# Optimization experiments

Measured on AMD Instinct MI355X. Metric: run time of the kernel, lower is better.

The kernel has to match this reference:

```python
import jax, jax.numpy as jnp
import numpy as np

GAMMA = 1.0

def setup_inputs() -> dict:
    key = jax.random.key(0)
    k1, k2 = jax.random.split(key)
    pred = jax.random.normal(k1, (8, 2048, 8), dtype=jnp.float32)
    target = jax.random.normal(k2, (8, 2048, 8), dtype=jnp.float32)
    return {"pred": pred, "target": target}

def reference(pred, target):
    # pairwise squared distances dist[b,i,j] = sum_f (pred[b,i,f]-target[b,j,f])^2
    # computed as ||p||^2 + ||t||^2 - 2 p.t to avoid materializing (B,L,L,F)
    p2 = jnp.sum(pred * pred, axis=-1)            # (B, L)
    t2 = jnp.sum(target * target, axis=-1)        # (B, L)
    pt = jnp.einsum('bif,bjf->bij', pred, target) # (B, L, L)
    distances = p2[:, :, None] + t2[:, None, :] - 2.0 * pt
    # soft-min over target positions: -gamma * logsumexp(-d/gamma)
    min_distances = -GAMMA * jax.nn.logsumexp(-distances / GAMMA, axis=-1)
    return jnp.mean(min_distances)
```

## Files before the change

kernel.cpp:

```cpp
#include <hip/hip_runtime.h>
#include <math.h>

#define BATCH 8
#define LEN   2048
#define FEAT  8
#define MROWS 64
#define THREADS 1024
#define JW    (LEN / 4)
#define NCHUNK (JW / 16)
#define NBLK  (BATCH * (LEN / MROWS))
#define LOG2E 1.4426950408889634f
#define LN2   0.6931471805599453f

typedef _Float16 f16x8 __attribute__((ext_vector_type(8)));
typedef float    f32x4 __attribute__((ext_vector_type(4)));

__device__ __forceinline__ float exp2_hw(float x) {
    float d; asm("v_exp_f32 %0, %1" : "=v"(d) : "v"(x)); return d;
}
__device__ __forceinline__ float log2_hw(float x) {
    float d; asm("v_log_f32 %0, %1" : "=v"(d) : "v"(x)); return d;
}

template <bool ATOMIC>
__global__ __launch_bounds__(THREADS, 4) void dtw_mfma(
    const float* __restrict__ pred, const float* __restrict__ target,
    float* __restrict__ partial_or_out)
{
    __shared__ f16x8 s_t16[LEN];
    __shared__ float s_mt2[LEN];

    const int tid = threadIdx.x;
    const int b   = blockIdx.x / (LEN / MROWS);
    const int rs  = blockIdx.x % (LEN / MROWS);
    const int w   = tid >> 6;
    const int rg  = w >> 2;
    const int jq  = w & 3;
    const int ln  = tid & 63;
    const int i0  = rs * MROWS + rg * 16;

    const float4* t4 = (const float4*)(target + (size_t)b * LEN * FEAT);
    #pragma unroll
    for (int u = 0; u < LEN / THREADS; ++u) {
        const int jj = u * THREADS + tid;
        float4 ta = t4[(size_t)jj * 2];
        float4 tb = t4[(size_t)jj * 2 + 1];
        f16x8 h;
        h[0] = (_Float16)ta.x; h[1] = (_Float16)ta.y;
        h[2] = (_Float16)ta.z; h[3] = (_Float16)ta.w;
        h[4] = (_Float16)tb.x; h[5] = (_Float16)tb.y;
        h[6] = (_Float16)tb.z; h[7] = (_Float16)tb.w;
        float t2 = 0.f;
        #pragma unroll
        for (int e = 0; e < 8; ++e) { float f = (float)h[e]; t2 += f * f; }
        s_t16[jj] = h;
        s_mt2[jj] = -LOG2E * t2;
    }

    f16x8 afrag;
    #pragma unroll
    for (int e = 0; e < 8; ++e) afrag[e] = (_Float16)0.f;
    float mp2_lane = 0.f;
    if (ln < 16) {
        const float4* p4 =
            (const float4*)(pred + ((size_t)b * LEN + i0 + ln) * FEAT);
        float4 a = p4[0], c = p4[1];
        f16x8 h;
        h[0] = (_Float16)a.x; h[1] = (_Float16)a.y;
        h[2] = (_Float16)a.z; h[3] = (_Float16)a.w;
        h[4] = (_Float16)c.x; h[5] = (_Float16)c.y;
        h[6] = (_Float16)c.z; h[7] = (_Float16)c.w;
        float p2 = 0.f;
        #pragma unroll
        for (int e = 0; e < 8; ++e) { float f = (float)h[e]; p2 += f * f; }
        #pragma unroll
        for (int e = 0; e < 8; ++e) afrag[e] = h[e] * (_Float16)2.0f;
        mp2_lane = -LOG2E * p2;
    }
    float m2r[4];
    #pragma unroll
    for (int r = 0; r < 4; ++r)
        m2r[r] = __shfl(mp2_lane, (ln >> 4) * 4 + r);

    __syncthreads();

    const int jbase = jq * JW;
    f32x4 acc = {0.f, 0.f, 0.f, 0.f};
    #pragma unroll 4
    for (int ch = 0; ch < NCHUNK; ++ch) {
        const int j0 = jbase + ch * 16;
        f16x8 bfrag;
        #pragma unroll
        for (int e = 0; e < 8; ++e) bfrag[e] = (_Float16)0.f;
        if (ln < 16) bfrag = s_t16[j0 + ln];
        float mt2c = s_mt2[j0 + (ln & 15)];
        f32x4 S = __builtin_amdgcn_mfma_f32_16x16x32_f16(
            afrag, bfrag, (f32x4){0.f, 0.f, 0.f, 0.f}, 0, 0, 0);
        #pragma unroll
        for (int r = 0; r < 4; ++r) {
            float x = fmaf(S[r], LOG2E, m2r[r] + mt2c);
            acc[r] += exp2_hw(x);
        }
    }

    #pragma unroll
    for (int m = 1; m < 16; m <<= 1) {
        #pragma unroll
        for (int r = 0; r < 4; ++r) acc[r] += __shfl_xor(acc[r], m);
    }

    __syncthreads();
    float* s_red = (float*)s_t16;
    if ((ln & 15) == 0) {
        #pragma unroll
        for (int r = 0; r < 4; ++r) {
            const int row = rg * 16 + (ln >> 4) * 4 + r;
            s_red[row * 4 + jq] = acc[r];
        }
    }
    __syncthreads();
    if (tid < 64) {
        float s = s_red[tid * 4] + s_red[tid * 4 + 1]
                + s_red[tid * 4 + 2] + s_red[tid * 4 + 3];
        float v = log2_hw(s);
        v += __shfl_xor(v, 1);
        v += __shfl_xor(v, 2);
        v += __shfl_xor(v, 4);
        v += __shfl_xor(v, 8);
        v += __shfl_xor(v, 16);
        v += __shfl_xor(v, 32);
        if (tid == 0) {
            float tot = -LN2 * v;
            if (ATOMIC) {
                atomicAdd(partial_or_out, tot * (1.0f / (BATCH * LEN)));
            } else {
                partial_or_out[blockIdx.x] = tot;
            }
        }
    }
}

__global__ __launch_bounds__(256) void dtw_reduce(
    const float* __restrict__ partial, float* __restrict__ out)
{
    __shared__ float s_w[4];
    const int tid = threadIdx.x;
    float v = partial[tid];
    v += __shfl_xor(v, 1);
    v += __shfl_xor(v, 2);
    v += __shfl_xor(v, 4);
    v += __shfl_xor(v, 8);
    v += __shfl_xor(v, 16);
    v += __shfl_xor(v, 32);
    if ((tid & 63) == 0) s_w[tid >> 6] = v;
    __syncthreads();
    if (tid == 0)
        out[0] = (s_w[0] + s_w[1] + s_w[2] + s_w[3]) * (1.0f / (BATCH * LEN));
}

extern "C" void kernel_launch(void* const* d_in, const int* in_sizes, int n_in,
                              void* d_out, int out_size, void* d_ws, size_t ws_size,
                              hipStream_t stream) {
    const float* pred   = (const float*)d_in[0];
    const float* target = (const float*)d_in[1];
    float* out = (float*)d_out;

    if (ws_size >= NBLK * sizeof(float)) {
        float* partial = (float*)d_ws;
        dtw_mfma<false><<<NBLK, THREADS, 0, stream>>>(pred, target, partial);
        dtw_reduce<<<1, 256, 0, stream>>>(partial, out);
    } else {
        hipMemsetAsync(d_out, 0, sizeof(float), stream);
        dtw_mfma<true><<<NBLK, THREADS, 0, stream>>>(pred, target, out);
    }
}
```

Before: 16.04 us.

## Reuse each target fragment across two MFMAs and factor the pred norm out of the exponent

Each wave now covers 32 pred rows with two MFMAs sharing one B fragment, over an eighth of the target range instead of a quarter. The 2*log2e scale is folded into the fp16 A fragment, so the per-element exponent argument drops from an fma plus add to a single add. The per-row pred-norm term is instead subtracted once after the log. It also fully unrolls the chunk loop and uses a dedicated shared reduction buffer, which removes one barrier. The risk is more registers and less stable results, since the exp2 argument no longer includes the -p2 shift and could overflow for rows with large norms.

```diff
diff --git a/kernel.cpp b/kernel.cpp
--- a/kernel.cpp
+++ b/kernel.cpp
@@ -6,11 +6,12 @@
 #define FEAT  8
 #define MROWS 64
 #define THREADS 1024
-#define JW    (LEN / 4)
-#define NCHUNK (JW / 16)
+#define JO    (LEN / 8)
+#define NCHUNK (JO / 16)
 #define NBLK  (BATCH * (LEN / MROWS))
 #define LOG2E 1.4426950408889634f
 #define LN2   0.6931471805599453f
+#define P2S   (2.0f * LOG2E)
 
 typedef _Float16 f16x8 __attribute__((ext_vector_type(8)));
 typedef float    f32x4 __attribute__((ext_vector_type(4)));
@@ -29,15 +30,19 @@
 {
     __shared__ f16x8 s_t16[LEN];
     __shared__ float s_mt2[LEN];
+    __shared__ float s_red[MROWS * 8];
+    __shared__ float s_qp[MROWS];
 
     const int tid = threadIdx.x;
     const int b   = blockIdx.x / (LEN / MROWS);
     const int rs  = blockIdx.x % (LEN / MROWS);
     const int w   = tid >> 6;
-    const int rg  = w >> 2;
-    const int jq  = w & 3;
+    const int rg  = w >> 3;
+    const int jo  = w & 7;
     const int ln  = tid & 63;
-    const int i0  = rs * MROWS + rg * 16;
+    const int col = ln & 15;
+    const int g   = ln >> 4;
+    const int i0  = rs * MROWS + rg * 32;
 
     const float4* t4 = (const float4*)(target + (size_t)b * LEN * FEAT);
     #pragma unroll
@@ -57,72 +62,80 @@
         s_mt2[jj] = -LOG2E * t2;
     }
 
-    f16x8 afrag;
+    f16x8 afrag0, afrag1;
     #pragma unroll
-    for (int e = 0; e < 8; ++e) afrag[e] = (_Float16)0.f;
-    float mp2_lane = 0.f;
-    if (ln < 16) {
-        const float4* p4 =
-            (const float4*)(pred + ((size_t)b * LEN + i0 + ln) * FEAT);
-        float4 a = p4[0], c = p4[1];
-        f16x8 h;
-        h[0] = (_Float16)a.x; h[1] = (_Float16)a.y;
-        h[2] = (_Float16)a.z; h[3] = (_Float16)a.w;
-        h[4] = (_Float16)c.x; h[5] = (_Float16)c.y;
-        h[6] = (_Float16)c.z; h[7] = (_Float16)c.w;
-        float p2 = 0.f;
+    for (int e = 0; e < 8; ++e) { afrag0[e] = (_Float16)0.f;
+                                  afrag1[e] = (_Float16)0.f; }
+    float qp0 = 0.f, qp1 = 0.f;
+    {
+        const float* pb = pred + ((size_t)b * LEN + i0 + col) * FEAT;
+        const float4* pA = (const float4*)pb;
+        const float4* pB = (const float4*)(pb + 16 * FEAT);
+        float4 a0 = pA[0], c0 = pA[1], a1 = pB[0], c1 = pB[1];
+        float f0[8] = {a0.x, a0.y, a0.z, a0.w, c0.x, c0.y, c0.z, c0.w};
+        float f1[8] = {a1.x, a1.y, a1.z, a1.w, c1.x, c1.y, c1.z, c1.w};
+        f16x8 r0, r1;
+        float e0 = 0.f, e1 = 0.f;
         #pragma unroll
-        for (int e = 0; e < 8; ++e) { float f = (float)h[e]; p2 += f * f; }
-        #pragma unroll
-        for (int e = 0; e < 8; ++e) afrag[e] = h[e] * (_Float16)2.0f;
-        mp2_lane = -LOG2E * p2;
+        for (int e = 0; e < 8; ++e) {
+            r0[e] = (_Float16)(P2S * f0[e]);
+            r1[e] = (_Float16)(P2S * f1[e]);
+            float x0 = (float)r0[e], x1 = (float)r1[e];
+            e0 += x0 * x0; e1 += x1 * x1;
+        }
+        qp0 = e0 * (0.25f / LOG2E);
+        qp1 = e1 * (0.25f / LOG2E);
+        if (g == 0) { afrag0 = r0; afrag1 = r1; }
+        if (jo == 0 && g == 0) {
+            s_qp[rg * 32 + col]      = qp0;
+            s_qp[rg * 32 + 16 + col] = qp1;
+        }
     }
-    float m2r[4];
-    #pragma unroll
-    for (int r = 0; r < 4; ++r)
-        m2r[r] = __shfl(mp2_lane, (ln >> 4) * 4 + r);
 
     __syncthreads();
 
-    const int jbase = jq * JW;
-    f32x4 acc = {0.f, 0.f, 0.f, 0.f};
-    #pragma unroll 4
+    const int jbase = jo * JO;
+    f32x4 acc0 = {0.f, 0.f, 0.f, 0.f};
+    f32x4 acc1 = {0.f, 0.f, 0.f, 0.f};
+    const f32x4 Z = {0.f, 0.f, 0.f, 0.f};
+    #pragma unroll
     for (int ch = 0; ch < NCHUNK; ++ch) {
         const int j0 = jbase + ch * 16;
-        f16x8 bfrag;
-        #pragma unroll
-        for (int e = 0; e < 8; ++e) bfrag[e] = (_Float16)0.f;
-        if (ln < 16) bfrag = s_t16[j0 + ln];
-        float mt2c = s_mt2[j0 + (ln & 15)];
-        f32x4 S = __builtin_amdgcn_mfma_f32_16x16x32_f16(
-            afrag, bfrag, (f32x4){0.f, 0.f, 0.f, 0.f}, 0, 0, 0);
+        f16x8 bfrag = s_t16[j0 + col];
+        float mt2c  = s_mt2[j0 + col];
+        f32x4 S0 = __builtin_amdgcn_mfma_f32_16x16x32_f16(
+            afrag0, bfrag, Z, 0, 0, 0);
+        f32x4 S1 = __builtin_amdgcn_mfma_f32_16x16x32_f16(
+            afrag1, bfrag, Z, 0, 0, 0);
         #pragma unroll
         for (int r = 0; r < 4; ++r) {
-            float x = fmaf(S[r], LOG2E, m2r[r] + mt2c);
-            acc[r] += exp2_hw(x);
+            acc0[r] += exp2_hw(S0[r] + mt2c);
+            acc1[r] += exp2_hw(S1[r] + mt2c);
         }
     }
 
     #pragma unroll
     for (int m = 1; m < 16; m <<= 1) {
         #pragma unroll
-        for (int r = 0; r < 4; ++r) acc[r] += __shfl_xor(acc[r], m);
+        for (int r = 0; r < 4; ++r) {
+            acc0[r] += __shfl_xor(acc0[r], m);
+            acc1[r] += __shfl_xor(acc1[r], m);
+        }
     }
-
-    __syncthreads();
-    float* s_red = (float*)s_t16;
-    if ((ln & 15) == 0) {
+    if (col == 0) {
         #pragma unroll
         for (int r = 0; r < 4; ++r) {
-            const int row = rg * 16 + (ln >> 4) * 4 + r;
-            s_red[row * 4 + jq] = acc[r];
+            s_red[(rg * 32 + g * 4 + r) * 8 + jo]      = acc0[r];
+            s_red[(rg * 32 + 16 + g * 4 + r) * 8 + jo] = acc1[r];
         }
     }
     __syncthreads();
-    if (tid < 64) {
-        float s = s_red[tid * 4] + s_red[tid * 4 + 1]
-                + s_red[tid * 4 + 2] + s_red[tid * 4 + 3];
-        float v = log2_hw(s);
+
+    if (tid < MROWS) {
+        float s = 0.f;
+        #pragma unroll
+        for (int q = 0; q < 8; ++q) s += s_red[tid * 8 + q];
+        float v = log2_hw(s) - s_qp[tid];
         v += __shfl_xor(v, 1);
         v += __shfl_xor(v, 2);
         v += __shfl_xor(v, 4);
```

After: 14.22 us, median of 2. -11.3%, faster.
